# Kernel optimization log

Measured on AMD Instinct MI355X. Metric: run time of the kernel, lower is better.

The kernel has to match this reference:

```python
import jax, jax.numpy as jnp
import numpy as np

S_MUL, V_MUL = 32, 16          # 32x0e + 16x1o
NODE_DIM = S_MUL + 3 * V_MUL   # 80
LATENT = 128
INV_SQRT3 = 1.0 / np.sqrt(3.0)          # wigner 3j (1,1,0) / (0,1,1) / (1,0,1) factor
C_SCALAR = np.float32(1.0 / np.sqrt(48.0))   # path_norm 'element': fan into 0e = 32*1 + 16*1
C_VECTOR = np.float32(np.sqrt(3.0 / 48.0))   # irrep dim 3 / fan 48 for 1o output


def setup_inputs() -> dict:
    rng = np.random.default_rng(0)
    B, n_atoms, radius = 2048, 32, 5.0
    N = B * n_atoms
    # atoms uniform in a 10A cube -> ~300 edges per 32-atom graph at r=5
    pos_g = rng.uniform(0.0, 10.0, size=(B, n_atoms, 3)).astype(np.float32)
    diff = pos_g[:, :, None, :] - pos_g[:, None, :, :]
    d2 = (diff * diff).sum(-1)
    mask = (d2 <= radius * radius) & (d2 > 0.0)   # same predicate as build_radius_graph
    b_idx, i_idx, j_idx = np.nonzero(mask)
    edge_index = np.stack([b_idx * n_atoms + i_idx, b_idx * n_atoms + j_idx]).astype(np.int32)
    pos = pos_g.reshape(N, 3)
    z = rng.integers(0, 100, size=N).astype(np.int32)
    batch = np.repeat(np.arange(B, dtype=np.int32), n_atoms)
    L = 3  # num_layers

    def w(*shape, scale=1.0):
        return jnp.asarray((rng.standard_normal(shape) * scale).astype(np.float32))

    return dict(
        pos=jnp.asarray(pos), z=jnp.asarray(z), batch=jnp.asarray(batch),
        edge_index=jnp.asarray(edge_index), num_graphs=B,
        emb=w(100, S_MUL),                      # nn.Embedding(100, 32) ~ N(0,1)
        W_s2n=w(S_MUL, S_MUL),                  # e3nn Linear 32x0e -> 32x0e path
        W1=w(L, S_MUL, S_MUL),                  # tp path 0e x 0e -> 0e
        W2=w(L, S_MUL, V_MUL),                  # tp path 0e x 1o -> 1o
        W3=w(L, V_MUL, V_MUL),                  # tp path 1o x 0e -> 1o
        W4=w(L, V_MUL, S_MUL),                  # tp path 1o x 1o -> 0e
        Ws=w(L, S_MUL, S_MUL),                  # e3nn Linear scalar block
        Wv=w(L, V_MUL, V_MUL),                  # e3nn Linear vector block
        Wr1=w(NODE_DIM, 256, scale=1.0 / np.sqrt(NODE_DIM)), br1=jnp.zeros((256,), jnp.float32),
        Wr2=w(256, LATENT, scale=1.0 / np.sqrt(256.0)), br2=jnp.zeros((LATENT,), jnp.float32),
    )


def _forward(pos, emb, W_s2n, W1, W2, W3, W4, Ws, Wv, Wr1, br1, Wr2, br2,
             z, batch, edge_index, num_graphs):
    N = pos.shape[0]
    src, dst = edge_index[0], edge_index[1]
    # atom embedding -> node irreps (only 0e->0e path exists; vectors start at 0)
    s = (emb[z] @ W_s2n) * np.float32(1.0 / np.sqrt(S_MUL))   # (N, 32)
    v = jnp.zeros((N, V_MUL, 3), pos.dtype)                   # (N, 16, 3)
    # spherical harmonics, normalize=True, 'component': Y0 = 1, Y1 = sqrt(3) * r_hat
    rij = pos[dst] - pos[src]                                 # (E, 3)
    sh1 = np.float32(np.sqrt(3.0)) * rij / jnp.linalg.norm(rij, axis=-1, keepdims=True)
    for l in range(W1.shape[0]):
        ss, vs = s[src], v[src]                               # gather (E,32), (E,16,3)
        # FullyConnectedTensorProduct(node, sh, node), uvw weights, sh0 == 1
        m_s = C_SCALAR * (jnp.einsum('eu,uw->ew', ss, W1[l])
                          + INV_SQRT3 * jnp.einsum('eui,ei,uw->ew', vs, sh1, W4[l]))
        m_v = (C_VECTOR * INV_SQRT3) * (jnp.einsum('eu,ei,uw->ewi', ss, sh1, W2[l])
                                        + jnp.einsum('eui,uw->ewi', vs, W3[l]))
        a_s = jax.ops.segment_sum(m_s, dst, num_segments=N)   # index_add_ scatter
        a_v = jax.ops.segment_sum(m_v, dst, num_segments=N)
        # e3nn Linear (per-irrep block, 1/sqrt(fan_in)) then relu on FULL feature (as in source)
        h_s = jax.nn.relu((a_s @ Ws[l]) * np.float32(1.0 / np.sqrt(S_MUL)))
        h_v = jax.nn.relu(jnp.einsum('nvi,vw->nwi', a_v, Wv[l]) * np.float32(1.0 / np.sqrt(V_MUL)))
        s, v = s + h_s, v + h_v                               # residual
    x = jnp.concatenate([s, v.reshape(N, V_MUL * 3)], axis=-1)  # (N, 80)
    hg = jax.ops.segment_sum(x, batch, num_segments=num_graphs) # sum-pool per graph
    return jax.nn.relu(hg @ Wr1 + br1) @ Wr2 + br2              # (B, latent)


def reference(pos, emb, W_s2n, W1, W2, W3, W4, Ws, Wv, Wr1, br1, Wr2, br2,
              z, batch, edge_index, num_graphs):
    return _forward(pos, emb, W_s2n, W1, W2, W3, W4, Ws, Wv, Wr1, br1, Wr2, br2,
                    z, batch, edge_index, num_graphs)
```

## Files before the change

kernel.cpp:

```cpp
#include <hip/hip_runtime.h>
#include <math.h>

typedef __attribute__((ext_vector_type(8))) short bf16x8;
typedef __attribute__((ext_vector_type(4))) float f32x4;

#define SQRT3F     1.7320508075688772f
#define SCALE_T    0.17677669529663687f
#define SCALE_M1   0.025515518153991442f
#define SCALE_M2   0.014731391274719739f
#define SCALE_M34  0.036084391824351615f

#define FSTR 40

__device__ __forceinline__ ushort f2bf(float f) {
    union { float f; unsigned u; } v; v.f = f;
    unsigned u = v.u;
    return (ushort)((u + 0x7FFFu + ((u >> 16) & 1u)) >> 16);
}
__device__ __forceinline__ float bf2f(ushort h) {
    union { unsigned u; float f; } v; v.u = ((unsigned)h) << 16;
    return v.f;
}
__device__ __forceinline__ unsigned cvtpk(float lo, float hi) {
    unsigned r;
    asm("v_cvt_pk_bf16_f32 %0, %1, %2" : "=v"(r) : "v"(lo), "v"(hi));
    return r;
}
__device__ __forceinline__ f32x4 mfma(bf16x8 a, bf16x8 b, f32x4 c) {
    return __builtin_amdgcn_mfma_f32_16x16x32_bf16(a, b, c, 0, 0, 0);
}
__device__ __forceinline__ bf16x8 frag2(f32x4 A, f32x4 B) {
    union { bf16x8 v; unsigned u[4]; } r;
    asm("v_cvt_pk_bf16_f32 %0, %4, %5\n\t"
        "v_cvt_pk_bf16_f32 %1, %6, %7\n\t"
        "v_cvt_pk_bf16_f32 %2, %8, %9\n\t"
        "v_cvt_pk_bf16_f32 %3, %10, %11\n\t"
        "s_nop 3"
        : "=&v"(r.u[0]), "=&v"(r.u[1]), "=&v"(r.u[2]), "=&v"(r.u[3])
        : "v"(A[0]), "v"(A[1]), "v"(A[2]), "v"(A[3]),
          "v"(B[0]), "v"(B[1]), "v"(B[2]), "v"(B[3]));
    return r.v;
}
__device__ __forceinline__ bf16x8 frag1z(f32x4 A) {
    union { bf16x8 v; unsigned u[4]; } r;
    asm("v_cvt_pk_bf16_f32 %0, %2, %3\n\t"
        "v_cvt_pk_bf16_f32 %1, %4, %5\n\t"
        "s_nop 3"
        : "=&v"(r.u[0]), "=&v"(r.u[1])
        : "v"(A[0]), "v"(A[1]), "v"(A[2]), "v"(A[3]));
    r.u[2] = 0u; r.u[3] = 0u;
    return r.v;
}
__device__ __forceinline__ void accRelu(f32x4 &S, f32x4 h) {
    S[0] += fmaxf(h[0], 0.f); S[1] += fmaxf(h[1], 0.f);
    S[2] += fmaxf(h[2], 0.f); S[3] += fmaxf(h[3], 0.f);
}

__global__ void prep_kernel(const float* __restrict__ emb,
                            const float* __restrict__ W_s2n,
                            const float* __restrict__ W1, const float* __restrict__ W2,
                            const float* __restrict__ W3, const float* __restrict__ W4,
                            const float* __restrict__ Ws, const float* __restrict__ Wv,
                            ushort* __restrict__ Tbf, ushort* __restrict__ Mbf)
{
    int idx = blockIdx.x * blockDim.x + threadIdx.x;
    if (idx < 3200) {
        int r = idx >> 5, c = idx & 31;
        float acc = 0.f;
        for (int k = 0; k < 32; ++k) acc += emb[r*32 + k] * W_s2n[k*32 + c];
        Tbf[idx] = f2bf(acc * SCALE_T);
        return;
    }
    idx -= 3200;
    if (idx < 3*48*64) {
        int lyr = idx / 3072, rem = idx % 3072;
        int row = rem >> 6, c = rem & 63;
        int kc = c >> 5, c5 = c & 31, kq2 = c5 >> 3, e = c5 & 7;
        int u = kc*32 + (e >> 2)*16 + kq2*4 + (e & 3);
        float val = 0.f;
        if (row < 32) {
            int w = row;
            if (u < 32) {
                float a = 0.f;
                for (int k = 0; k < 32; ++k)
                    a += W1[lyr*1024 + u*32 + k] * Ws[lyr*1024 + k*32 + w];
                val = a * SCALE_M1;
            } else if (u < 48) {
                int uu = u - 32; float a = 0.f;
                for (int k = 0; k < 32; ++k)
                    a += W4[lyr*512 + uu*32 + k] * Ws[lyr*1024 + k*32 + w];
                val = a * SCALE_M2;
            }
        } else {
            int w = row - 32;
            if (u < 32) {
                float a = 0.f;
                for (int k = 0; k < 16; ++k)
                    a += W2[lyr*512 + u*16 + k] * Wv[lyr*256 + k*16 + w];
                val = a * SCALE_M34;
            } else if (u < 48) {
                int uu = u - 32; float a = 0.f;
                for (int k = 0; k < 16; ++k)
                    a += W3[lyr*256 + uu*16 + k] * Wv[lyr*256 + k*16 + w];
                val = a * SCALE_M34;
            }
        }
        Mbf[lyr*3072 + row*64 + c] = f2bf(val);
    }
}

__global__ __launch_bounds__(256)
void gnn_kernel(const float* __restrict__ pos, const int* __restrict__ z,
                const ushort* __restrict__ Tbf, const ushort* __restrict__ Mbf,
                const float* __restrict__ Wr1, const float* __restrict__ br1,
                const float* __restrict__ Wr2, const float* __restrict__ br2,
                float* __restrict__ out, int B)
{
    __shared__ __align__(16) char smem[26880];
    ushort* featA = (ushort*)smem;
    float*  hgl   = (float*)(smem + 25600);
    float*  h1    = (float*)smem;
    float*  red   = (float*)(smem + 4096);

    const int tid = threadIdx.x;
    const int wv = tid >> 6, l = tid & 63;
    const int g  = blockIdx.x*4 + wv;
    ushort* F  = featA + wv*80*FSTR;
    const int ln = l & 15, kq = l >> 4;

    {
        int n = l & 31, h = l >> 5;
        int zg = z[g*32 + n];
        uint4 t0 = *(const uint4*)(Tbf + zg*32 + h*16);
        uint4 t1 = *(const uint4*)(Tbf + zg*32 + h*16 + 8);
        unsigned ua[8] = {t0.x, t0.y, t0.z, t0.w, t1.x, t1.y, t1.z, t1.w};
        #pragma unroll
        for (int q = 0; q < 8; ++q) {
            F[(h*16 + 2*q    )*FSTR + n] = (ushort)ua[q];
            F[(h*16 + 2*q + 1)*FSTR + n] = (ushort)(ua[q] >> 16);
        }
    }

    f32x4 Ss[2][2];
    f32x4 Sv[2][3];
    #pragma unroll
    for (int mt = 0; mt < 2; ++mt) {
        #pragma unroll
        for (int wt = 0; wt < 2; ++wt) {
            uint2 d = *(const uint2*)&F[(wt*16 + ln)*FSTR + mt*16 + kq*4];
            Ss[mt][wt][0] = bf2f((ushort)(d.x      ));
            Ss[mt][wt][1] = bf2f((ushort)(d.x >> 16));
            Ss[mt][wt][2] = bf2f((ushort)(d.y      ));
            Ss[mt][wt][3] = bf2f((ushort)(d.y >> 16));
        }
        #pragma unroll
        for (int i = 0; i < 3; ++i)
            Sv[mt][i] = (f32x4){0.f, 0.f, 0.f, 0.f};
    }

    bf16x8 adjf[4][2];
    {
        #pragma unroll
        for (int nt = 0; nt < 2; ++nt) {
            int ng = g*32 + nt*16 + ln;
            float px = pos[3*ng], py = pos[3*ng+1], pz = pos[3*ng+2];
            union { bf16x8 v; ushort s[8]; } o[4];
            #pragma unroll
            for (int jj = 0; jj < 8; ++jj) {
                int j = g*32 + ((jj >> 2) << 4) + kq*4 + (jj & 3);
                float dx = __fsub_rn(px, pos[3*j]);
                float dy = __fsub_rn(py, pos[3*j+1]);
                float dz = __fsub_rn(pz, pos[3*j+2]);
                float d2 = __fadd_rn(__fadd_rn(__fmul_rn(dx,dx), __fmul_rn(dy,dy)),
                                     __fmul_rn(dz,dz));
                bool on = (d2 <= 25.0f) && (d2 > 0.0f);
                float rinv = on ? rsqrtf(d2) * SQRT3F : 0.f;
                o[0].s[jj] = on ? (ushort)0x3F80 : (ushort)0;
                o[1].s[jj] = f2bf(dx * rinv);
                o[2].s[jj] = f2bf(dy * rinv);
                o[3].s[jj] = f2bf(dz * rinv);
            }
            #pragma unroll
            for (int w = 0; w < 4; ++w) adjf[w][nt] = o[w].v;
        }
    }

    const f32x4 z4 = {0.f, 0.f, 0.f, 0.f};

    for (int lay = 0; lay < 3; ++lay) {
        const ushort* Mg = Mbf + lay*3072;
        bf16x8 fs0 = frag2(Ss[0][0], Ss[1][0]);
        bf16x8 fs1 = frag2(Ss[0][1], Ss[1][1]);
        bf16x8 fv0 = frag2(Sv[0][0], Sv[1][0]);
        bf16x8 fv1 = frag2(Sv[0][1], Sv[1][1]);
        bf16x8 fv2 = frag2(Sv[0][2], Sv[1][2]);
        bf16x8 bmS0[2], bmS1[2], bmV[2];
        #pragma unroll
        for (int kc = 0; kc < 2; ++kc) {
            bmS0[kc] = *(const bf16x8*)&Mg[(     ln)*64 + kc*32 + kq*8];
            bmS1[kc] = *(const bf16x8*)&Mg[(16 + ln)*64 + kc*32 + kq*8];
            bmV [kc] = *(const bf16x8*)&Mg[(32 + ln)*64 + kc*32 + kq*8];
        }

        bf16x8 agf[2][2];

        #pragma unroll
        for (int nt = 0; nt < 2; ++nt) {
            f32x4 T0 = mfma(fs0, adjf[0][nt], z4);
            f32x4 T1 = mfma(fs1, adjf[0][nt], z4);
            f32x4 T2 = mfma(fv2, adjf[3][nt], z4);
            T2 = mfma(fv1, adjf[2][nt], T2);
            T2 = mfma(fv0, adjf[1][nt], T2);
            agf[nt][0] = frag2(T0, T1);
            agf[nt][1] = frag1z(T2);
        }
        f32x4 hs[2][2] = {{z4, z4}, {z4, z4}};
        #pragma unroll
        for (int kc = 0; kc < 2; ++kc)
            #pragma unroll
            for (int mt = 0; mt < 2; ++mt) {
                hs[mt][0] = mfma(agf[mt][kc], bmS0[kc], hs[mt][0]);
                hs[mt][1] = mfma(agf[mt][kc], bmS1[kc], hs[mt][1]);
            }
        #pragma unroll
        for (int mt = 0; mt < 2; ++mt)
            #pragma unroll
            for (int wt = 0; wt < 2; ++wt)
                accRelu(Ss[mt][wt], hs[mt][wt]);

        #pragma unroll
        for (int i = 0; i < 3; ++i) {
            bf16x8 fvi = (i == 0) ? fv0 : (i == 1) ? fv1 : fv2;
            #pragma unroll
            for (int nt = 0; nt < 2; ++nt) {
                f32x4 T0 = mfma(fs0, adjf[1+i][nt], z4);
                f32x4 T1 = mfma(fs1, adjf[1+i][nt], z4);
                f32x4 T2 = mfma(fvi, adjf[0][nt], z4);
                agf[nt][0] = frag2(T0, T1);
                agf[nt][1] = frag1z(T2);
            }
            f32x4 hv[2] = {z4, z4};
            #pragma unroll
            for (int kc = 0; kc < 2; ++kc)
                #pragma unroll
                for (int mt = 0; mt < 2; ++mt)
                    hv[mt] = mfma(agf[mt][kc], bmV[kc], hv[mt]);
            #pragma unroll
            for (int mt = 0; mt < 2; ++mt)
                accRelu(Sv[mt][i], hv[mt]);
        }
    }

    #pragma unroll
    for (int mt = 0; mt < 2; ++mt) {
        #pragma unroll
        for (int wt = 0; wt < 2; ++wt) {
            uint2 w;
            w.x = cvtpk(Ss[mt][wt][0], Ss[mt][wt][1]);
            w.y = cvtpk(Ss[mt][wt][2], Ss[mt][wt][3]);
            *(uint2*)&F[(wt*16 + ln)*FSTR + mt*16 + kq*4] = w;
        }
        #pragma unroll
        for (int i = 0; i < 3; ++i) {
            uint2 w;
            w.x = cvtpk(Sv[mt][i][0], Sv[mt][i][1]);
            w.y = cvtpk(Sv[mt][i][2], Sv[mt][i][3]);
            *(uint2*)&F[(32 + i*16 + ln)*FSTR + mt*16 + kq*4] = w;
        }
    }

    for (int f = l; f < 80; f += 64) {
        const ushort* row;
        if (f < 32) row = &F[f*FSTR];
        else { int c = f - 32, w = c/3, i = c - 3*w; row = &F[(32 + i*16 + w)*FSTR]; }
        const uint* r32 = (const uint*)row;
        float acc = 0.f;
        #pragma unroll
        for (int q = 0; q < 16; ++q) {
            uint u = r32[q];
            acc += bf2f((ushort)u) + bf2f((ushort)(u >> 16));
        }
        hgl[wv*80 + f] = acc;
    }
    __syncthreads();

    {
        const int w = tid;
        float acc0 = br1[w];
        float acc1 = acc0, acc2 = acc0, acc3 = acc0;
        #pragma unroll 4
        for (int f = 0; f < 80; ++f) {
            float wvv = Wr1[f*256 + w];
            acc0 = fmaf(hgl[0*80 + f], wvv, acc0);
            acc1 = fmaf(hgl[1*80 + f], wvv, acc1);
            acc2 = fmaf(hgl[2*80 + f], wvv, acc2);
            acc3 = fmaf(hgl[3*80 + f], wvv, acc3);
        }
        h1[0*256 + w] = fmaxf(acc0, 0.f);
        h1[1*256 + w] = fmaxf(acc1, 0.f);
        h1[2*256 + w] = fmaxf(acc2, 0.f);
        h1[3*256 + w] = fmaxf(acc3, 0.f);
    }
    __syncthreads();
    {
        const int g0 = blockIdx.x * 4;
        const int w2 = tid & 127, kh = tid >> 7;
        const float4* h1v = (const float4*)h1;
        float s0 = 0.f, s1 = 0.f, s2 = 0.f, s3 = 0.f;
        #pragma unroll 2
        for (int k4 = kh*32; k4 < kh*32 + 32; ++k4) {
            float4 hA = h1v[0*64 + k4];
            float4 hB = h1v[1*64 + k4];
            float4 hC = h1v[2*64 + k4];
            float4 hD = h1v[3*64 + k4];
            int k = k4 * 4;
            float m0 = Wr2[(size_t)(k+0)*128 + w2];
            float m1 = Wr2[(size_t)(k+1)*128 + w2];
            float m2 = Wr2[(size_t)(k+2)*128 + w2];
            float m3 = Wr2[(size_t)(k+3)*128 + w2];
            s0 = fmaf(hA.x,m0, fmaf(hA.y,m1, fmaf(hA.z,m2, fmaf(hA.w,m3, s0))));
            s1 = fmaf(hB.x,m0, fmaf(hB.y,m1, fmaf(hB.z,m2, fmaf(hB.w,m3, s1))));
            s2 = fmaf(hC.x,m0, fmaf(hC.y,m1, fmaf(hC.z,m2, fmaf(hC.w,m3, s2))));
            s3 = fmaf(hD.x,m0, fmaf(hD.y,m1, fmaf(hD.z,m2, fmaf(hD.w,m3, s3))));
        }
        if (kh) {
            red[0*128 + w2] = s0; red[1*128 + w2] = s1;
            red[2*128 + w2] = s2; red[3*128 + w2] = s3;
        }
        __syncthreads();
        if (!kh) {
            float b = br2[w2];
            out[(size_t)(g0+0)*128 + w2] = s0 + red[0*128 + w2] + b;
            out[(size_t)(g0+1)*128 + w2] = s1 + red[1*128 + w2] + b;
            out[(size_t)(g0+2)*128 + w2] = s2 + red[2*128 + w2] + b;
            out[(size_t)(g0+3)*128 + w2] = s3 + red[3*128 + w2] + b;
        }
    }
}

extern "C" void kernel_launch(void* const* d_in, const int* in_sizes, int n_in,
                              void* d_out, int out_size, void* d_ws, size_t ws_size,
                              hipStream_t stream)
{
    const float* pos   = (const float*)d_in[0];
    const int*   z     = (const int*)d_in[1];
    const float* emb   = (const float*)d_in[5];
    const float* W_s2n = (const float*)d_in[6];
    const float* W1    = (const float*)d_in[7];
    const float* W2    = (const float*)d_in[8];
    const float* W3    = (const float*)d_in[9];
    const float* W4    = (const float*)d_in[10];
    const float* Ws    = (const float*)d_in[11];
    const float* Wv    = (const float*)d_in[12];
    const float* Wr1   = (const float*)d_in[13];
    const float* br1   = (const float*)d_in[14];
    const float* Wr2   = (const float*)d_in[15];
    const float* br2   = (const float*)d_in[16];
    float* out = (float*)d_out;

    const int B = out_size / 128;

    char* p = (char*)d_ws;
    ushort* Tbf = (ushort*)p;  p += 6400;
    ushort* Mbf = (ushort*)p;  p += 18432;

    const int prep_total = 3200 + 3*48*64;
    prep_kernel<<<(prep_total + 255) / 256, 256, 0, stream>>>(
        emb, W_s2n, W1, W2, W3, W4, Ws, Wv, Tbf, Mbf);

    gnn_kernel<<<B / 4, 256, 0, stream>>>(pos, z, Tbf, Mbf,
                                          Wr1, br1, Wr2, br2, out, B);
}
```

Baseline: 109.9 us.

## Process two graphs per wavefront and eight graphs per block

Each wavefront now handles two 32-atom graphs instead of one, so a block covers eight graphs and the grid is halved. The two graphs' MFMA chains are interleaved, which adds independent work to hide MFMA latency and spreads the Mbf weight fragment loads and the readout-MLP weight reads (Wr1/Wr2) over twice as many graphs. In exchange the kernel uses twice the shared memory and many more registers (duplicated state and adjacency fragments). That can lower occupancy, and with B=2048 the grid shrinks to 256 blocks, which may leave compute units underfilled.

```diff
diff --git a/kernel.cpp b/kernel.cpp
--- a/kernel.cpp
+++ b/kernel.cpp
@@ -116,21 +116,22 @@
                 const float* __restrict__ Wr2, const float* __restrict__ br2,
                 float* __restrict__ out, int B)
 {
-    __shared__ __align__(16) char smem[26880];
+    __shared__ __align__(16) char smem[53760];
     ushort* featA = (ushort*)smem;
-    float*  hgl   = (float*)(smem + 25600);
+    float*  hgl   = (float*)(smem + 51200);
     float*  h1    = (float*)smem;
-    float*  red   = (float*)(smem + 4096);
+    float*  red   = (float*)(smem + 8192);
 
     const int tid = threadIdx.x;
     const int wv = tid >> 6, l = tid & 63;
-    const int g  = blockIdx.x*4 + wv;
-    ushort* F  = featA + wv*80*FSTR;
+    const int gbase = blockIdx.x*8 + wv*2;
     const int ln = l & 15, kq = l >> 4;
 
-    {
+    #pragma unroll
+    for (int p = 0; p < 2; ++p) {
+        ushort* F = featA + (wv*2 + p)*80*FSTR;
         int n = l & 31, h = l >> 5;
-        int zg = z[g*32 + n];
+        int zg = z[(gbase + p)*32 + n];
         uint4 t0 = *(const uint4*)(Tbf + zg*32 + h*16);
         uint4 t1 = *(const uint4*)(Tbf + zg*32 + h*16 + 8);
         unsigned ua[8] = {t0.x, t0.y, t0.z, t0.w, t1.x, t1.y, t1.z, t1.w};
@@ -141,33 +142,38 @@
         }
     }
 
-    f32x4 Ss[2][2];
-    f32x4 Sv[2][3];
+    f32x4 Ss[2][2][2];
+    f32x4 Sv[2][2][3];
     #pragma unroll
-    for (int mt = 0; mt < 2; ++mt) {
-        #pragma unroll
-        for (int wt = 0; wt < 2; ++wt) {
-            uint2 d = *(const uint2*)&F[(wt*16 + ln)*FSTR + mt*16 + kq*4];
-            Ss[mt][wt][0] = bf2f((ushort)(d.x      ));
-            Ss[mt][wt][1] = bf2f((ushort)(d.x >> 16));
-            Ss[mt][wt][2] = bf2f((ushort)(d.y      ));
-            Ss[mt][wt][3] = bf2f((ushort)(d.y >> 16));
-        }
-        #pragma unroll
-        for (int i = 0; i < 3; ++i)
-            Sv[mt][i] = (f32x4){0.f, 0.f, 0.f, 0.f};
-    }
-
-    bf16x8 adjf[4][2];
-    {
+    for (int p = 0; p < 2; ++p) {
+        ushort* F = featA + (wv*2 + p)*80*FSTR;
+        #pragma unroll
+        for (int mt = 0; mt < 2; ++mt) {
+            #pragma unroll
+            for (int wt = 0; wt < 2; ++wt) {
+                uint2 d = *(const uint2*)&F[(wt*16 + ln)*FSTR + mt*16 + kq*4];
+                Ss[p][mt][wt][0] = bf2f((ushort)(d.x      ));
+                Ss[p][mt][wt][1] = bf2f((ushort)(d.x >> 16));
+                Ss[p][mt][wt][2] = bf2f((ushort)(d.y      ));
+                Ss[p][mt][wt][3] = bf2f((ushort)(d.y >> 16));
+            }
+            #pragma unroll
+            for (int i = 0; i < 3; ++i)
+                Sv[p][mt][i] = (f32x4){0.f, 0.f, 0.f, 0.f};
+        }
+    }
+
+    bf16x8 adjf[2][4][2];
+    #pragma unroll
+    for (int p = 0; p < 2; ++p) {
         #pragma unroll
         for (int nt = 0; nt < 2; ++nt) {
-            int ng = g*32 + nt*16 + ln;
+            int ng = (gbase + p)*32 + nt*16 + ln;
             float px = pos[3*ng], py = pos[3*ng+1], pz = pos[3*ng+2];
             union { bf16x8 v; ushort s[8]; } o[4];
             #pragma unroll
             for (int jj = 0; jj < 8; ++jj) {
-                int j = g*32 + ((jj >> 2) << 4) + kq*4 + (jj & 3);
+                int j = (gbase + p)*32 + ((jj >> 2) << 4) + kq*4 + (jj & 3);
                 float dx = __fsub_rn(px, pos[3*j]);
                 float dy = __fsub_rn(py, pos[3*j+1]);
                 float dz = __fsub_rn(pz, pos[3*j+2]);
@@ -181,7 +187,7 @@
                 o[3].s[jj] = f2bf(dz * rinv);
             }
             #pragma unroll
-            for (int w = 0; w < 4; ++w) adjf[w][nt] = o[w].v;
+            for (int w = 0; w < 4; ++w) adjf[p][w][nt] = o[w].v;
         }
     }
 
@@ -189,11 +195,6 @@
 
     for (int lay = 0; lay < 3; ++lay) {
         const ushort* Mg = Mbf + lay*3072;
-        bf16x8 fs0 = frag2(Ss[0][0], Ss[1][0]);
-        bf16x8 fs1 = frag2(Ss[0][1], Ss[1][1]);
-        bf16x8 fv0 = frag2(Sv[0][0], Sv[1][0]);
-        bf16x8 fv1 = frag2(Sv[0][1], Sv[1][1]);
-        bf16x8 fv2 = frag2(Sv[0][2], Sv[1][2]);
         bf16x8 bmS0[2], bmS1[2], bmV[2];
         #pragma unroll
         for (int kc = 0; kc < 2; ++kc) {
@@ -201,139 +202,175 @@
             bmS1[kc] = *(const bf16x8*)&Mg[(16 + ln)*64 + kc*32 + kq*8];
             bmV [kc] = *(const bf16x8*)&Mg[(32 + ln)*64 + kc*32 + kq*8];
         }
-
-        bf16x8 agf[2][2];
-
-        #pragma unroll
-        for (int nt = 0; nt < 2; ++nt) {
-            f32x4 T0 = mfma(fs0, adjf[0][nt], z4);
-            f32x4 T1 = mfma(fs1, adjf[0][nt], z4);
-            f32x4 T2 = mfma(fv2, adjf[3][nt], z4);
-            T2 = mfma(fv1, adjf[2][nt], T2);
-            T2 = mfma(fv0, adjf[1][nt], T2);
-            agf[nt][0] = frag2(T0, T1);
-            agf[nt][1] = frag1z(T2);
-        }
-        f32x4 hs[2][2] = {{z4, z4}, {z4, z4}};
-        #pragma unroll
-        for (int kc = 0; kc < 2; ++kc)
-            #pragma unroll
-            for (int mt = 0; mt < 2; ++mt) {
-                hs[mt][0] = mfma(agf[mt][kc], bmS0[kc], hs[mt][0]);
-                hs[mt][1] = mfma(agf[mt][kc], bmS1[kc], hs[mt][1]);
-            }
-        #pragma unroll
-        for (int mt = 0; mt < 2; ++mt)
-            #pragma unroll
-            for (int wt = 0; wt < 2; ++wt)
-                accRelu(Ss[mt][wt], hs[mt][wt]);
+        bf16x8 fs0[2], fs1[2], fv0[2], fv1[2], fv2[2];
+        #pragma unroll
+        for (int p = 0; p < 2; ++p) {
+            fs0[p] = frag2(Ss[p][0][0], Ss[p][1][0]);
+            fs1[p] = frag2(Ss[p][0][1], Ss[p][1][1]);
+            fv0[p] = frag2(Sv[p][0][0], Sv[p][1][0]);
+            fv1[p] = frag2(Sv[p][0][1], Sv[p][1][1]);
+            fv2[p] = frag2(Sv[p][0][2], Sv[p][1][2]);
+        }
+
+        bf16x8 agf[2][2][2];
+
+        #pragma unroll
+        for (int p = 0; p < 2; ++p)
+            #pragma unroll
+            for (int nt = 0; nt < 2; ++nt) {
+                f32x4 T0 = mfma(fs0[p], adjf[p][0][nt], z4);
+                f32x4 T1 = mfma(fs1[p], adjf[p][0][nt], z4);
+                f32x4 T2 = mfma(fv2[p], adjf[p][3][nt], z4);
+                T2 = mfma(fv1[p], adjf[p][2][nt], T2);
+                T2 = mfma(fv0[p], adjf[p][1][nt], T2);
+                agf[p][nt][0] = frag2(T0, T1);
+                agf[p][nt][1] = frag1z(T2);
+            }
+        {
+            f32x4 hs[2][2][2];
+            #pragma unroll
+            for (int p = 0; p < 2; ++p)
+                #pragma unroll
+                for (int mt = 0; mt < 2; ++mt) {
+                    hs[p][mt][0] = z4; hs[p][mt][1] = z4;
+                }
+            #pragma unroll
+            for (int kc = 0; kc < 2; ++kc)
+                #pragma unroll
+                for (int p = 0; p < 2; ++p)
+                    #pragma unroll
+                    for (int mt = 0; mt < 2; ++mt) {
+                        hs[p][mt][0] = mfma(agf[p][mt][kc], bmS0[kc], hs[p][mt][0]);
+                        hs[p][mt][1] = mfma(agf[p][mt][kc], bmS1[kc], hs[p][mt][1]);
+                    }
+            #pragma unroll
+            for (int p = 0; p < 2; ++p)
+                #pragma unroll
+                for (int mt = 0; mt < 2; ++mt) {
+                    accRelu(Ss[p][mt][0], hs[p][mt][0]);
+                    accRelu(Ss[p][mt][1], hs[p][mt][1]);
+                }
+        }
 
         #pragma unroll
         for (int i = 0; i < 3; ++i) {
-            bf16x8 fvi = (i == 0) ? fv0 : (i == 1) ? fv1 : fv2;
-            #pragma unroll
-            for (int nt = 0; nt < 2; ++nt) {
-                f32x4 T0 = mfma(fs0, adjf[1+i][nt], z4);
-                f32x4 T1 = mfma(fs1, adjf[1+i][nt], z4);
-                f32x4 T2 = mfma(fvi, adjf[0][nt], z4);
-                agf[nt][0] = frag2(T0, T1);
-                agf[nt][1] = frag1z(T2);
-            }
-            f32x4 hv[2] = {z4, z4};
+            #pragma unroll
+            for (int p = 0; p < 2; ++p) {
+                bf16x8 fvi = (i == 0) ? fv0[p] : (i == 1) ? fv1[p] : fv2[p];
+                #pragma unroll
+                for (int nt = 0; nt < 2; ++nt) {
+                    f32x4 T0 = mfma(fs0[p], adjf[p][1+i][nt], z4);
+                    f32x4 T1 = mfma(fs1[p], adjf[p][1+i][nt], z4);
+                    f32x4 T2 = mfma(fvi, adjf[p][0][nt], z4);
+                    agf[p][nt][0] = frag2(T0, T1);
+                    agf[p][nt][1] = frag1z(T2);
+                }
+            }
+            f32x4 hv[2][2];
+            #pragma unroll
+            for (int p = 0; p < 2; ++p) { hv[p][0] = z4; hv[p][1] = z4; }
             #pragma unroll
             for (int kc = 0; kc < 2; ++kc)
                 #pragma unroll
+                for (int p = 0; p < 2; ++p)
+                    #pragma unroll
+                    for (int mt = 0; mt < 2; ++mt)
+                        hv[p][mt] = mfma(agf[p][mt][kc], bmV[kc], hv[p][mt]);
+            #pragma unroll
+            for (int p = 0; p < 2; ++p)
+                #pragma unroll
                 for (int mt = 0; mt < 2; ++mt)
-                    hv[mt] = mfma(agf[mt][kc], bmV[kc], hv[mt]);
-            #pragma unroll
-            for (int mt = 0; mt < 2; ++mt)
-                accRelu(Sv[mt][i], hv[mt]);
+                    accRelu(Sv[p][mt][i], hv[p][mt]);
         }
     }
 
     #pragma unroll
-    for (int mt = 0; mt < 2; ++mt) {
-        #pragma unroll
-        for (int wt = 0; wt < 2; ++wt) {
-            uint2 w;
-            w.x = cvtpk(Ss[mt][wt][0], Ss[mt][wt][1]);
-            w.y = cvtpk(Ss[mt][wt][2], Ss[mt][wt][3]);
-            *(uint2*)&F[(wt*16 + ln)*FSTR + mt*16 + kq*4] = w;
-        }
-        #pragma unroll
-        for (int i = 0; i < 3; ++i) {
-            uint2 w;
-            w.x = cvtpk(Sv[mt][i][0], Sv[mt][i][1]);
-            w.y = cvtpk(Sv[mt][i][2], Sv[mt][i][3]);
-            *(uint2*)&F[(32 + i*16 + ln)*FSTR + mt*16 + kq*4] = w;
-        }
-    }
-
-    for (int f = l; f < 80; f += 64) {
-        const ushort* row;
-        if (f < 32) row = &F[f*FSTR];
-        else { int c = f - 32, w = c/3, i = c - 3*w; row = &F[(32 + i*16 + w)*FSTR]; }
-        const uint* r32 = (const uint*)row;
-        float acc = 0.f;
-        #pragma unroll
-        for (int q = 0; q < 16; ++q) {
-            uint u = r32[q];
-            acc += bf2f((ushort)u) + bf2f((ushort)(u >> 16));
-        }
-        hgl[wv*80 + f] = acc;
+    for (int p = 0; p < 2; ++p) {
+        ushort* F = featA + (wv*2 + p)*80*FSTR;
+        #pragma unroll
+        for (int mt = 0; mt < 2; ++mt) {
+            #pragma unroll
+            for (int wt = 0; wt < 2; ++wt) {
+                uint2 w;
+                w.x = cvtpk(Ss[p][mt][wt][0], Ss[p][mt][wt][1]);
+                w.y = cvtpk(Ss[p][mt][wt][2], Ss[p][mt][wt][3]);
+                *(uint2*)&F[(wt*16 + ln)*FSTR + mt*16 + kq*4] = w;
+            }
+            #pragma unroll
+            for (int i = 0; i < 3; ++i) {
+                uint2 w;
+                w.x = cvtpk(Sv[p][mt][i][0], Sv[p][mt][i][1]);
+                w.y = cvtpk(Sv[p][mt][i][2], Sv[p][mt][i][3]);
+                *(uint2*)&F[(32 + i*16 + ln)*FSTR + mt*16 + kq*4] = w;
+            }
+        }
+    }
+
+    #pragma unroll
+    for (int p = 0; p < 2; ++p) {
+        ushort* F = featA + (wv*2 + p)*80*FSTR;
+        for (int f = l; f < 80; f += 64) {
+            const ushort* row;
+            if (f < 32) row = &F[f*FSTR];
+            else { int c = f - 32, w = c/3, i = c - 3*w; row = &F[(32 + i*16 + w)*FSTR]; }
+            const uint* r32 = (const uint*)row;
+            float acc = 0.f;
+            #pragma unroll
+            for (int q = 0; q < 16; ++q) {
+                uint u = r32[q];
+                acc += bf2f((ushort)u) + bf2f((ushort)(u >> 16));
+            }
+            hgl[(wv*2 + p)*80 + f] = acc;
+        }
     }
     __syncthreads();
 
     {
         const int w = tid;
-        float acc0 = br1[w];
-        float acc1 = acc0, acc2 = acc0, acc3 = acc0;
+        float acc[8];
+        #pragma unroll
+        for (int gg = 0; gg < 8; ++gg) acc[gg] = br1[w];
         #pragma unroll 4
         for (int f = 0; f < 80; ++f) {
             float wvv = Wr1[f*256 + w];
-            acc0 = fmaf(hgl[0*80 + f], wvv, acc0);
-            acc1 = fmaf(hgl[1*80 + f], wvv, acc1);
-            acc2 = fmaf(hgl[2*80 + f], wvv, acc2);
-            acc3 = fmaf(hgl[3*80 + f], wvv, acc3);
-        }
-        h1[0*256 + w] = fmaxf(acc0, 0.f);
-        h1[1*256 + w] = fmaxf(acc1, 0.f);
-        h1[2*256 + w] = fmaxf(acc2, 0.f);
-        h1[3*256 + w] = fmaxf(acc3, 0.f);
+            #pragma unroll
+            for (int gg = 0; gg < 8; ++gg)
+                acc[gg] = fmaf(hgl[gg*80 + f], wvv, acc[gg]);
+        }
+        #pragma unroll
+        for (int gg = 0; gg < 8; ++gg)
+            h1[gg*256 + w] = fmaxf(acc[gg], 0.f);
     }
     __syncthreads();
     {
-        const int g0 = blockIdx.x * 4;
+        const int g0 = blockIdx.x * 8;
         const int w2 = tid & 127, kh = tid >> 7;
         const float4* h1v = (const float4*)h1;
-        float s0 = 0.f, s1 = 0.f, s2 = 0.f, s3 = 0.f;
-        #pragma unroll 2
+        float s[8];
+        #pragma unroll
+        for (int gg = 0; gg < 8; ++gg) s[gg] = 0.f;
         for (int k4 = kh*32; k4 < kh*32 + 32; ++k4) {
-            float4 hA = h1v[0*64 + k4];
-            float4 hB = h1v[1*64 + k4];
-            float4 hC = h1v[2*64 + k4];
-            float4 hD = h1v[3*64 + k4];
             int k = k4 * 4;
             float m0 = Wr2[(size_t)(k+0)*128 + w2];
             float m1 = Wr2[(size_t)(k+1)*128 + w2];
             float m2 = Wr2[(size_t)(k+2)*128 + w2];
             float m3 = Wr2[(size_t)(k+3)*128 + w2];
-            s0 = fmaf(hA.x,m0, fmaf(hA.y,m1, fmaf(hA.z,m2, fmaf(hA.w,m3, s0))));
-            s1 = fmaf(hB.x,m0, fmaf(hB.y,m1, fmaf(hB.z,m2, fmaf(hB.w,m3, s1))));
-            s2 = fmaf(hC.x,m0, fmaf(hC.y,m1, fmaf(hC.z,m2, fmaf(hC.w,m3, s2))));
-            s3 = fmaf(hD.x,m0, fmaf(hD.y,m1, fmaf(hD.z,m2, fmaf(hD.w,m3, s3))));
+            #pragma unroll
+            for (int gg = 0; gg < 8; ++gg) {
+                float4 hh = h1v[gg*64 + k4];
+                s[gg] = fmaf(hh.x,m0, fmaf(hh.y,m1, fmaf(hh.z,m2, fmaf(hh.w,m3, s[gg]))));
+            }
         }
         if (kh) {
-            red[0*128 + w2] = s0; red[1*128 + w2] = s1;
-            red[2*128 + w2] = s2; red[3*128 + w2] = s3;
+            #pragma unroll
+            for (int gg = 0; gg < 8; ++gg) red[gg*128 + w2] = s[gg];
         }
         __syncthreads();
         if (!kh) {
             float b = br2[w2];
-            out[(size_t)(g0+0)*128 + w2] = s0 + red[0*128 + w2] + b;
-            out[(size_t)(g0+1)*128 + w2] = s1 + red[1*128 + w2] + b;
-            out[(size_t)(g0+2)*128 + w2] = s2 + red[2*128 + w2] + b;
-            out[(size_t)(g0+3)*128 + w2] = s3 + red[3*128 + w2] + b;
+            #pragma unroll
+            for (int gg = 0; gg < 8; ++gg)
+                out[(size_t)(g0+gg)*128 + w2] = s[gg] + red[gg*128 + w2] + b;
         }
     }
 }
@@ -368,6 +405,6 @@
     prep_kernel<<<(prep_total + 255) / 256, 256, 0, stream>>>(
         emb, W_s2n, W1, W2, W3, W4, Ws, Wv, Tbf, Mbf);
 
-    gnn_kernel<<<B / 4, 256, 0, stream>>>(pos, z, Tbf, Mbf,
+    gnn_kernel<<<B / 8, 256, 0, stream>>>(pos, z, Tbf, Mbf,
                                           Wr1, br1, Wr2, br2, out, B);
 }
```

New measurement: 117.7 us. +7.1%, slower.
